# Kernel optimization log

Hardware: AMD Instinct MI355X
Metric: run time of the kernel (lower is better)

The kernel has to match this reference:

```python
import jax, jax.numpy as jnp
import numpy as np
import math

B, S, E = 2, 2048, 1024
H, HD = 16, 64
FF = 4 * E
EPS = float(jnp.finfo(jnp.float32).eps)  # torch nn.RMSNorm default eps


def setup_inputs() -> dict:
    key = jax.random.key(0)
    ks = jax.random.split(key, 20)
    sd = 0.02
    inp = {
        "x": jax.random.normal(ks[0], (B, S, E), jnp.float32),
        "wq": jax.random.normal(ks[1], (E, H * HD), jnp.float32) * sd,
        "bq": jnp.zeros((H * HD,), jnp.float32),
        "wk": jax.random.normal(ks[2], (E, HD), jnp.float32) * sd,
        "bk": jnp.zeros((HD,), jnp.float32),
        "wv": jax.random.normal(ks[3], (E, HD), jnp.float32) * sd,
        "bv": jnp.zeros((HD,), jnp.float32),
        "wo": jax.random.normal(ks[4], (H * HD, E), jnp.float32) * sd,
        "bo": jnp.zeros((E,), jnp.float32),
        "wg": jax.random.normal(ks[5], (E, FF), jnp.float32) * sd,
        "bg": jnp.zeros((FF,), jnp.float32),
        "wu": jax.random.normal(ks[6], (E, FF), jnp.float32) * sd,
        "bu": jnp.zeros((FF,), jnp.float32),
        "wd": jax.random.normal(ks[7], (FF, E), jnp.float32) * sd,
        "bd": jnp.zeros((E,), jnp.float32),
        "g1": jnp.ones((E,), jnp.float32),
        "g2": jnp.ones((E,), jnp.float32),
    }
    return inp


def rmsnorm(x, g):
    ms = jnp.mean(jnp.square(x), axis=-1, keepdims=True)
    return x * jax.lax.rsqrt(ms + EPS) * g


def apply_rope(t):
    # t: [B, H, S, D]; llama-style rotate-half, theta=10000, start_pos=0
    d = t.shape[-1]
    half = d // 2
    inv_freq = 1.0 / (10000.0 ** (jnp.arange(half, dtype=jnp.float32) / half))
    pos = jnp.arange(t.shape[2], dtype=jnp.float32)
    ang = pos[:, None] * inv_freq[None, :]  # [S, half]
    cos, sin = jnp.cos(ang), jnp.sin(ang)
    t1, t2 = t[..., :half], t[..., half:]
    return jnp.concatenate([t1 * cos - t2 * sin, t1 * sin + t2 * cos], axis=-1)


def decoder_fwd(x, wq, bq, wk, bk, wv, bv, wo, bo, wg, bg, wu, bu, wd, bd, g1, g2):
    residual = x
    h = rmsnorm(x, g1)
    # MQA projections: H query heads, 1 shared K/V head
    q = (h @ wq + bq).reshape(B, S, H, HD).transpose(0, 2, 1, 3)  # [B,H,S,D]
    k = (h @ wk + bk)[:, None]                                    # [B,1,S,D]
    v = (h @ wv + bv)                                             # [B,S,D]
    q = apply_rope(q)
    k = apply_rope(k)[:, 0]                                       # [B,S,D]
    scores = jnp.einsum("bhqd,bkd->bhqk", q, k) / math.sqrt(HD)
    causal = jnp.tril(jnp.ones((S, S), dtype=bool))
    scores = jnp.where(causal, scores, -jnp.inf)
    attn = jax.nn.softmax(scores, axis=-1)
    out = jnp.einsum("bhqk,bkd->bhqd", attn, v)
    out = out.transpose(0, 2, 1, 3).reshape(B, S, H * HD)
    x = (out @ wo + bo) + residual
    residual = x
    h = rmsnorm(x, g2)
    gated = jax.nn.gelu(h @ wg + bg, approximate=False)  # torch GELU is exact erf
    up = h @ wu + bu
    x = (up * gated) @ wd + bd
    return x + residual


def reference(x, wq, bq, wk, bk, wv, bv, wo, bo, wg, bg, wu, bu, wd, bd, g1, g2):
    return decoder_fwd(x, wq, bq, wk, bk, wv, bv, wo, bo, wg, bg, wu, bu, wd, bd, g1, g2)
```

## Files before the change

### kernel.cpp

```cpp
#include <hip/hip_runtime.h>
#include <hip/hip_bf16.h>
#include <math.h>

#define BB 2
#define SS 2048
#define EE 1024
#define HH 16
#define HD 64
#define FFF 4096
#define MROWS (BB * SS)
#define EPS_F 1.1920929e-7f
#define NQKV 1152

typedef __hip_bfloat16 bf16;
typedef __attribute__((ext_vector_type(8))) short short8;
typedef __attribute__((ext_vector_type(4))) short short4v;
typedef __attribute__((ext_vector_type(4))) float floatx4;

typedef const __attribute__((address_space(1))) void* gas_t;
typedef __attribute__((address_space(3))) void* las_t;

#define BAR __builtin_amdgcn_s_barrier()
#define WLG do { asm volatile("s_waitcnt lgkmcnt(0)" ::: "memory"); \
                 __builtin_amdgcn_sched_barrier(0); } while (0)
#define VMC(N) asm volatile("s_waitcnt vmcnt(" #N ")" ::: "memory")

__global__ __launch_bounds__(256) void rmsnorm_kernel(const float* __restrict__ x,
                                                      const float* __restrict__ g,
                                                      bf16* __restrict__ out,
                                                      int cols) {
    int row = blockIdx.x;
    const float* xr = x + (size_t)row * cols;
    float ss = 0.0f;
    for (int c = threadIdx.x; c < cols; c += 256) {
        float v = xr[c];
        ss += v * v;
    }
    for (int off = 32; off > 0; off >>= 1) ss += __shfl_xor(ss, off, 64);
    __shared__ float red[4];
    int wave = threadIdx.x >> 6;
    if ((threadIdx.x & 63) == 0) red[wave] = ss;
    __syncthreads();
    float tot = red[0] + red[1] + red[2] + red[3];
    float rs = rsqrtf(tot / (float)cols + EPS_F);
    bf16* orow = out + (size_t)row * cols;
    for (int c = threadIdx.x; c < cols; c += 256) {
        orow[c] = __float2bfloat16(xr[c] * rs * g[c]);
    }
}

__device__ __forceinline__ void transpose_tile32(const float* __restrict__ W,
                                                 bf16* __restrict__ Wt,
                                                 int K, int N, int bx, int by,
                                                 int tid, float (*t)[33]) {
    int n0 = bx * 32, k0 = by * 32;
    int tx = tid & 31, ty = tid >> 5;
#pragma unroll
    for (int i = 0; i < 4; ++i) {
        int kk = ty + i * 8;
        t[kk][tx] = W[(size_t)(k0 + kk) * N + n0 + tx];
    }
    __syncthreads();
#pragma unroll
    for (int i = 0; i < 4; ++i) {
        int nn = ty + i * 8;
        Wt[(size_t)(n0 + nn) * K + k0 + tx] = __float2bfloat16(t[tx][nn]);
    }
}

__global__ __launch_bounds__(256) void prep_weights_kernel(
        const float* __restrict__ wq, const float* __restrict__ wk,
        const float* __restrict__ wv, const float* __restrict__ wo,
        const float* __restrict__ bq, const float* __restrict__ bk,
        const float* __restrict__ bv,
        bf16* __restrict__ wqkvT, bf16* __restrict__ woT,
        float* __restrict__ bqkv, float* __restrict__ ct, float* __restrict__ st) {
    __shared__ float t[32][33];
    int bid = blockIdx.x, tid = threadIdx.x;
    if (bid < 1024) {
        transpose_tile32(wq, wqkvT, EE, EE, bid & 31, bid >> 5, tid, t);
    } else if (bid < 1088) {
        int b2 = bid - 1024;
        transpose_tile32(wk, wqkvT + (size_t)1024 * EE, EE, HD, b2 & 1, b2 >> 1, tid, t);
    } else if (bid < 1152) {
        int b2 = bid - 1088;
        transpose_tile32(wv, wqkvT + (size_t)1088 * EE, EE, HD, b2 & 1, b2 >> 1, tid, t);
    } else if (bid < 2176) {
        int b2 = bid - 1152;
        transpose_tile32(wo, woT, EE, EE, b2 & 31, b2 >> 5, tid, t);
    } else if (bid < 2432) {
        int idx = (bid - 2176) * 256 + tid;
        int i = idx & 31, s = idx >> 5;
        float inv = powf(10000.0f, -(float)i / 32.0f);
        float ang = (float)s * inv;
        ct[idx] = cosf(ang);
        st[idx] = sinf(ang);
    } else {
        int tt = (bid - 2432) * 256 + tid;
        if (tt < NQKV) {
            float v;
            if (tt < 1024)      v = bq[tt];
            else if (tt < 1088) v = bk[tt - 1024];
            else                v = bv[tt - 1088];
            bqkv[tt] = v;
        }
    }
}

__global__ __launch_bounds__(256) void ffn_weights_kernel(
        const float* __restrict__ wg, const float* __restrict__ wu,
        const float* __restrict__ wd,
        bf16* __restrict__ wgT, bf16* __restrict__ wuT, bf16* __restrict__ wdT) {
    __shared__ float t[32][33];
    int bid = blockIdx.x, tid = threadIdx.x;
    if (bid < 4096) {
        transpose_tile32(wg, wgT, EE, FFF, bid & 127, bid >> 7, tid, t);
    } else if (bid < 8192) {
        int b2 = bid - 4096;
        transpose_tile32(wu, wuT, EE, FFF, b2 & 127, b2 >> 7, tid, t);
    } else {
        int b2 = bid - 8192;
        transpose_tile32(wd, wdT, FFF, EE, b2 & 31, b2 >> 5, tid, t);
    }
}

#define GK 64

__global__ __launch_bounds__(256) void gemm_qkv_kernel(
        const bf16* __restrict__ A, const bf16* __restrict__ Bt,
        const float* __restrict__ bias,
        const float* __restrict__ ct, const float* __restrict__ st,
        bf16* __restrict__ qout, bf16* __restrict__ kout,
        bf16* __restrict__ vout, int K) {
    __shared__ short As[128 * GK];
    __shared__ short Bs[128 * GK];
    int tid = threadIdx.x;
    int wave = tid >> 6, lane = tid & 63;
    int wm = (wave >> 1) * 64, wn = (wave & 1) * 64;
    int row0 = blockIdx.y * 128, col0 = blockIdx.x * 128;
    int lr = lane & 15, lq = lane >> 4;

    int srow = wave * 32 + (lane >> 3);
    int scol = (lane & 7) * 8;
    const bf16* Abase = A + (size_t)(row0 + srow) * K + scol;
    const bf16* Bbase = Bt + (size_t)(col0 + srow) * K + scol;

    floatx4 acc[4][4];
#pragma unroll
    for (int mi = 0; mi < 4; ++mi)
#pragma unroll
        for (int ni = 0; ni < 4; ++ni)
            acc[mi][ni] = (floatx4){0.f, 0.f, 0.f, 0.f};

    for (int k0 = 0; k0 < K; k0 += GK) {
        __syncthreads();
#pragma unroll
        for (int c = 0; c < 4; ++c) {
            __builtin_amdgcn_global_load_lds(
                (gas_t)(Abase + (size_t)(c * 8) * K + k0),
                (las_t)&As[(wave * 32 + c * 8) * GK], 16, 0, 0);
            __builtin_amdgcn_global_load_lds(
                (gas_t)(Bbase + (size_t)(c * 8) * K + k0),
                (las_t)&Bs[(wave * 32 + c * 8) * GK], 16, 0, 0);
        }
        __syncthreads();
#pragma unroll
        for (int ks = 0; ks < GK; ks += 32) {
            short8 af[4], bfr[4];
#pragma unroll
            for (int mi = 0; mi < 4; ++mi)
                af[mi] = *(const short8*)&As[(wm + mi * 16 + lr) * GK + ks + lq * 8];
#pragma unroll
            for (int ni = 0; ni < 4; ++ni)
                bfr[ni] = *(const short8*)&Bs[(wn + ni * 16 + lr) * GK + ks + lq * 8];
#pragma unroll
            for (int mi = 0; mi < 4; ++mi)
#pragma unroll
                for (int ni = 0; ni < 4; ++ni)
                    acc[mi][ni] = __builtin_amdgcn_mfma_f32_16x16x32_bf16(
                        af[mi], bfr[ni], acc[mi][ni], 0, 0, 0);
        }
    }

    int hcol = col0 + wn;
    if (hcol < 1088) {
        bool isQ = hcol < 1024;
#pragma unroll
        for (int mi = 0; mi < 4; ++mi) {
#pragma unroll
            for (int ni = 0; ni < 2; ++ni) {
                int i = ni * 16 + lr;
                float b1 = bias[hcol + i];
                float b2 = bias[hcol + i + 32];
#pragma unroll
                for (int r = 0; r < 4; ++r) {
                    int gr = row0 + wm + mi * 16 + lq * 4 + r;
                    int s = gr & (SS - 1);
                    float c  = ct[s * 32 + i];
                    float sn = st[s * 32 + i];
                    float t1 = acc[mi][ni][r] + b1;
                    float t2 = acc[mi][ni + 2][r] + b2;
                    float o1 = t1 * c - t2 * sn;
                    float o2 = t1 * sn + t2 * c;
                    if (isQ) {
                        qout[(size_t)gr * 1024 + hcol + i]      = __float2bfloat16(o1 * 0.125f);
                        qout[(size_t)gr * 1024 + hcol + i + 32] = __float2bfloat16(o2 * 0.125f);
                    } else {
                        kout[(size_t)gr * 64 + i]      = __float2bfloat16(o1);
                        kout[(size_t)gr * 64 + i + 32] = __float2bfloat16(o2);
                    }
                }
            }
        }
    } else {
#pragma unroll
        for (int mi = 0; mi < 4; ++mi)
#pragma unroll
            for (int ni = 0; ni < 4; ++ni) {
                int vcol = ni * 16 + lr;
                float bv_ = bias[1088 + vcol];
#pragma unroll
                for (int r = 0; r < 4; ++r) {
                    int gr = row0 + wm + mi * 16 + lq * 4 + r;
                    vout[(size_t)gr * 64 + vcol] = __float2bfloat16(acc[mi][ni][r] + bv_);
                }
            }
    }
}

__global__ __launch_bounds__(256) void gemm_n64_kernel(
        const bf16* __restrict__ A, const bf16* __restrict__ Bt,
        const float* __restrict__ bias, const float* __restrict__ aux,
        float* __restrict__ C, int M, int N, int K) {
    __shared__ short As[128 * GK];
    __shared__ short Bs[64 * GK];
    int tid = threadIdx.x;
    int wave = tid >> 6, lane = tid & 63;
    int wm = wave * 32;
    int row0 = blockIdx.y * 128, col0 = blockIdx.x * 64;
    int lr = lane & 15, lq = lane >> 4;

    int srow = (lane >> 3);
    int scol = (lane & 7) * 8;
    const bf16* Abase = A + (size_t)(row0 + wave * 32 + srow) * K + scol;
    const bf16* Bbase = Bt + (size_t)(col0 + wave * 16 + srow) * K + scol;

    floatx4 acc[2][4];
#pragma unroll
    for (int mi = 0; mi < 2; ++mi)
#pragma unroll
        for (int ni = 0; ni < 4; ++ni)
            acc[mi][ni] = (floatx4){0.f, 0.f, 0.f, 0.f};

    for (int k0 = 0; k0 < K; k0 += GK) {
        __syncthreads();
#pragma unroll
        for (int c = 0; c < 4; ++c)
            __builtin_amdgcn_global_load_lds(
                (gas_t)(Abase + (size_t)(c * 8) * K + k0),
                (las_t)&As[(wave * 32 + c * 8) * GK], 16, 0, 0);
#pragma unroll
        for (int c = 0; c < 2; ++c)
            __builtin_amdgcn_global_load_lds(
                (gas_t)(Bbase + (size_t)(c * 8) * K + k0),
                (las_t)&Bs[(wave * 16 + c * 8) * GK], 16, 0, 0);
        __syncthreads();
#pragma unroll
        for (int ks = 0; ks < GK; ks += 32) {
            short8 af[2], bfr[4];
#pragma unroll
            for (int mi = 0; mi < 2; ++mi)
                af[mi] = *(const short8*)&As[(wm + mi * 16 + lr) * GK + ks + lq * 8];
#pragma unroll
            for (int ni = 0; ni < 4; ++ni)
                bfr[ni] = *(const short8*)&Bs[(ni * 16 + lr) * GK + ks + lq * 8];
#pragma unroll
            for (int mi = 0; mi < 2; ++mi)
#pragma unroll
                for (int ni = 0; ni < 4; ++ni)
                    acc[mi][ni] = __builtin_amdgcn_mfma_f32_16x16x32_bf16(
                        af[mi], bfr[ni], acc[mi][ni], 0, 0, 0);
        }
    }

#pragma unroll
    for (int mi = 0; mi < 2; ++mi) {
#pragma unroll
        for (int ni = 0; ni < 4; ++ni) {
            int gc = col0 + ni * 16 + lr;
            float bv = bias[gc];
#pragma unroll
            for (int r = 0; r < 4; ++r) {
                int gr = row0 + wm + mi * 16 + lq * 4 + r;
                size_t idx = (size_t)gr * N + gc;
                C[idx] = acc[mi][ni][r] + bv + aux[idx];
            }
        }
    }
}

#define FFN_RD_A(KH, MH) \
    { const short* Ap = &Ab[buf][KH][0]; \
      af[0] = *(const short8*)&Ap[(wr * 128 + ((MH) * 4 + 0) * 16 + lr) * 32 + cs8]; \
      af[1] = *(const short8*)&Ap[(wr * 128 + ((MH) * 4 + 1) * 16 + lr) * 32 + cs8]; \
      af[2] = *(const short8*)&Ap[(wr * 128 + ((MH) * 4 + 2) * 16 + lr) * 32 + cs8]; \
      af[3] = *(const short8*)&Ap[(wr * 128 + ((MH) * 4 + 3) * 16 + lr) * 32 + cs8]; }

#define FFN_RD_B(KH) \
    { const short* Bp = &Bb[buf][KH][0]; \
      gf[0] = *(const short8*)&Bp[(wc * 32 + lr) * 32 + cs8]; \
      gf[1] = *(const short8*)&Bp[(wc * 32 + 16 + lr) * 32 + cs8]; \
      uf[0] = *(const short8*)&Bp[4096 + (wc * 32 + lr) * 32 + cs8]; \
      uf[1] = *(const short8*)&Bp[4096 + (wc * 32 + 16 + lr) * 32 + cs8]; }

#define FFN_MM(MH) \
    __builtin_amdgcn_s_setprio(1); \
    { _Pragma("unroll") for (int mi = 0; mi < 4; ++mi) { \
        ag[(MH) * 4 + mi][0] = __builtin_amdgcn_mfma_f32_16x16x32_bf16(af[mi], gf[0], ag[(MH) * 4 + mi][0], 0, 0, 0); \
        ag[(MH) * 4 + mi][1] = __builtin_amdgcn_mfma_f32_16x16x32_bf16(af[mi], gf[1], ag[(MH) * 4 + mi][1], 0, 0, 0); \
        au[(MH) * 4 + mi][0] = __builtin_amdgcn_mfma_f32_16x16x32_bf16(af[mi], uf[0], au[(MH) * 4 + mi][0], 0, 0, 0); \
        au[(MH) * 4 + mi][1] = __builtin_amdgcn_mfma_f32_16x16x32_bf16(af[mi], uf[1], au[(MH) * 4 + mi][1], 0, 0, 0); } } \
    __builtin_amdgcn_s_setprio(0);

__global__ __launch_bounds__(512, 2) void gemm_ffn_kernel(
        const bf16* __restrict__ A, const bf16* __restrict__ Bg,
        const bf16* __restrict__ Bu, const float* __restrict__ biasg,
        const float* __restrict__ biasu, bf16* __restrict__ C, int K) {
    __shared__ short Ab[2][2][8192];
    __shared__ short Bb[2][2][8192];

    const int tid = threadIdx.x;
    const int w = tid >> 6, lane = tid & 63;
    const int wr = w >> 2, wc = w & 3;
    const int lr = lane & 15, quad = lane >> 4;
    const int row0 = blockIdx.y * 256, col0 = blockIdx.x * 128;
    const int NT = K >> 6;
    const int cs8 = (quad ^ ((lr >> 1) & 3)) * 8;

    const int sr = tid >> 2;
    const int scs = (((tid & 3) ^ ((tid >> 3) & 3))) * 8;

    auto stageA = [&](short* dst, int kcol) {
        __builtin_amdgcn_global_load_lds(
            (gas_t)(A + (size_t)(row0 + sr) * K + kcol + scs),
            (las_t)(dst + tid * 8), 16, 0, 0);
        __builtin_amdgcn_global_load_lds(
            (gas_t)(A + (size_t)(row0 + 128 + sr) * K + kcol + scs),
            (las_t)(dst + 4096 + tid * 8), 16, 0, 0);
    };
    auto stageB = [&](short* dst, int kcol) {
        __builtin_amdgcn_global_load_lds(
            (gas_t)(Bg + (size_t)(col0 + sr) * K + kcol + scs),
            (las_t)(dst + tid * 8), 16, 0, 0);
        __builtin_amdgcn_global_load_lds(
            (gas_t)(Bu + (size_t)(col0 + sr) * K + kcol + scs),
            (las_t)(dst + 4096 + tid * 8), 16, 0, 0);
    };

    floatx4 ag[8][2], au[8][2];
#pragma unroll
    for (int mi = 0; mi < 8; ++mi)
#pragma unroll
        for (int ni = 0; ni < 2; ++ni) {
            ag[mi][ni] = (floatx4){0.f, 0.f, 0.f, 0.f};
            au[mi][ni] = (floatx4){0.f, 0.f, 0.f, 0.f};
        }

    stageA(&Ab[0][0][0], 0);
    stageB(&Bb[0][0][0], 0);
    stageA(&Ab[0][1][0], 32);
    stageB(&Bb[0][1][0], 32);
    stageA(&Ab[1][0][0], 64);
    stageB(&Bb[1][0][0], 64);
    VMC(8);
    BAR;

    for (int k = 0; k < NT; ++k) {
        const int buf = k & 1;
        short8 gf[2], uf[2];
        {
            short8 af[4];
            FFN_RD_A(0, 0)
            FFN_RD_B(0)
            if (k + 1 < NT) stageA(&Ab[buf ^ 1][1][0], (k + 1) * 64 + 32);
            BAR; WLG;
            FFN_MM(0)
            BAR;
        }
        {
            short8 af[4];
            FFN_RD_A(0, 1)
            if (k + 1 < NT) stageB(&Bb[buf ^ 1][1][0], (k + 1) * 64 + 32);
            BAR; WLG;
            FFN_MM(1)
            if (k < NT - 1) { VMC(8); } else { VMC(0); }
            BAR;
        }
        {
            short8 af[4];
            FFN_RD_A(1, 0)
            FFN_RD_B(1)
            if (k + 2 < NT) stageA(&Ab[buf][0][0], (k + 2) * 64);
            BAR; WLG;
            FFN_MM(0)
            BAR;
        }
        {
            short8 af[4];
            FFN_RD_A(1, 1)
            if (k + 2 < NT) stageB(&Bb[buf][0][0], (k + 2) * 64);
            BAR; WLG;
            FFN_MM(1)
            if (k < NT - 2) { VMC(8); } else if (k == NT - 2) { VMC(4); }
            BAR;
        }
    }

#pragma unroll
    for (int mi = 0; mi < 8; ++mi) {
#pragma unroll
        for (int ni = 0; ni < 2; ++ni) {
            int gc = col0 + wc * 32 + ni * 16 + lr;
            float bg_ = biasg[gc], bu_ = biasu[gc];
#pragma unroll
            for (int r = 0; r < 4; ++r) {
                int gr = row0 + wr * 128 + mi * 16 + quad * 4 + r;
                float g = ag[mi][ni][r] + bg_;
                float u = au[mi][ni][r] + bu_;
                float v = 0.5f * g * (1.0f + erff(g * 0.70710678118654752f)) * u;
                C[(size_t)gr * FFF + gc] = __float2bfloat16(v);
            }
        }
    }
}

__global__ __launch_bounds__(256) void prep_v_kernel(const bf16* __restrict__ vb,
                                                     bf16* __restrict__ vtb) {
    __shared__ short t[64][65];
    int s0 = blockIdx.x * 64, b = blockIdx.y;
    int tid = threadIdx.x;
    const short* vs = (const short*)vb;
    short* vd = (short*)vtb;
    for (int i = tid; i < 4096; i += 256) {
        int s = i >> 6, d = i & 63;
        t[d][s] = vs[((size_t)(b * SS + s0 + s)) * 64 + d];
    }
    __syncthreads();
    for (int i = tid; i < 4096; i += 256) {
        int d = i >> 6, sl = i & 63;
        vd[((size_t)(b * 64 + d)) * SS + s0 + sl] = t[d][sl];
    }
}

#define PST 68
#define SM_SHIFT 6.0f

__global__ __launch_bounds__(256, 3) void attn_mfma_kernel(
        const bf16* __restrict__ q, const bf16* __restrict__ kb,
        const bf16* __restrict__ vt,
        float* __restrict__ O0p, float* __restrict__ O1p,
        float* __restrict__ l0p, float* __restrict__ l1p) {
    __shared__ short Kb_s[2][64 * 64];
    __shared__ short Vb_s[2][64 * 64];
    __shared__ short Ps[4][16 * PST];

    int h = blockIdx.y, b = blockIdx.z;
    int px = blockIdx.x >> 1, half = blockIdx.x & 1;
    int tid = threadIdx.x, w = tid >> 6, lane = tid & 63;
    int lr = lane & 15, quad = lane >> 4;
    int rsw = lane & 7;

    float* __restrict__ Op = half ? O1p : O0p;
    float* __restrict__ lp = half ? l1p : l0p;

    const bf16* kbB = kb + (size_t)b * SS * 64;
    const bf16* vtB = vt + (size_t)b * 64 * SS;

    int st_sub = lane >> 3;
    int st_col = ((lane & 7) ^ st_sub) << 3;

    auto stage_tile = [&](int nxt, int j0s) {
#pragma unroll
        for (int i = 0; i < 2; ++i) {
            int rr = i * 32 + w * 8 + st_sub;
            __builtin_amdgcn_global_load_lds(
                (gas_t)(kbB + (size_t)(j0s + rr) * 64 + st_col),
                (las_t)&Kb_s[nxt][(i * 256 + w * 64) * 8], 16, 0, 0);
            __builtin_amdgcn_global_load_lds(
                (gas_t)(vtB + (size_t)rr * SS + j0s + st_col),
                (las_t)&Vb_s[nxt][(i * 256 + w * 64) * 8], 16, 0, 0);
        }
    };

    for (int pass = 0; pass < 2; ++pass) {
        int qt = (pass == 0) ? px : (SS / 64 - 1 - px);
        int q0 = qt * 64;

        const bf16* qrow = q + ((size_t)(b * SS + q0 + w * 16 + lr)) * (HH * HD) + h * HD;
        short8 qf0 = *(const short8*)(qrow + quad * 8);
        short8 qf1 = *(const short8*)(qrow + 32 + quad * 8);

        int n  = qt + 1;
        int n0 = (n + 1) >> 1;
        int tlo = half ? n0 : 0;
        int thi = half ? n  : n0;

        floatx4 O[4];
#pragma unroll
        for (int ni = 0; ni < 4; ++ni) O[ni] = (floatx4){0.f, 0.f, 0.f, 0.f};
        float lrow[4] = {0.f, 0.f, 0.f, 0.f};

        int cur = 0;
        if (tlo < thi) stage_tile(0, tlo * 64);
        __syncthreads();

        for (int t = tlo; t < thi; ++t) {
            if (t + 1 < thi) stage_tile(cur ^ 1, (t + 1) * 64);

            int j0 = t * 64;

            floatx4 S[4];
#pragma unroll
            for (int ni = 0; ni < 4; ++ni) S[ni] = (floatx4){0.f, 0.f, 0.f, 0.f};
#pragma unroll
            for (int ni = 0; ni < 4; ++ni) {
                const short* Kc = &Kb_s[cur][(ni * 16 + lr) * 64];
                short8 b0 = *(const short8*)&Kc[(quad ^ rsw) * 8];
                short8 b1 = *(const short8*)&Kc[((quad ^ rsw) ^ 4) * 8];
                S[ni] = __builtin_amdgcn_mfma_f32_16x16x32_bf16(qf0, b0, S[ni], 0, 0, 0);
                S[ni] = __builtin_amdgcn_mfma_f32_16x16x32_bf16(qf1, b1, S[ni], 0, 0, 0);
            }

            short8 vf[8];
#pragma unroll
            for (int ni = 0; ni < 4; ++ni) {
                const short* Vc = &Vb_s[cur][(ni * 16 + lr) * 64];
                vf[2 * ni]     = *(const short8*)&Vc[(quad ^ rsw) * 8];
                vf[2 * ni + 1] = *(const short8*)&Vc[((quad ^ rsw) ^ 4) * 8];
            }

            if (t == qt) {
                int rowg = q0 + w * 16 + quad * 4;
#pragma unroll
                for (int ni = 0; ni < 4; ++ni) {
                    int colg = j0 + ni * 16 + lr;
#pragma unroll
                    for (int r = 0; r < 4; ++r)
                        if (colg > rowg + r) S[ni][r] = -3.0e38f;
                }
            }

#pragma unroll
            for (int ni = 0; ni < 4; ++ni)
#pragma unroll
                for (int r = 0; r < 4; ++r)
                    S[ni][r] = __expf(S[ni][r] - SM_SHIFT);
#pragma unroll
            for (int r = 0; r < 4; ++r)
                lrow[r] += S[0][r] + S[1][r] + S[2][r] + S[3][r];

#pragma unroll
            for (int ni = 0; ni < 4; ++ni)
#pragma unroll
                for (int r = 0; r < 4; ++r) {
                    bf16 pb = __float2bfloat16(S[ni][r]);
                    Ps[w][(quad * 4 + r) * PST + ni * 16 + lr] = *(short*)&pb;
                }
            short4v a0 = *(const short4v*)&Ps[w][lr * PST + quad * 8];
            short4v a1 = *(const short4v*)&Ps[w][lr * PST + quad * 8 + 4];
            short4v a2 = *(const short4v*)&Ps[w][lr * PST + 32 + quad * 8];
            short4v a3 = *(const short4v*)&Ps[w][lr * PST + 32 + quad * 8 + 4];
            short8 p0 = __builtin_shufflevector(a0, a1, 0, 1, 2, 3, 4, 5, 6, 7);
            short8 p1 = __builtin_shufflevector(a2, a3, 0, 1, 2, 3, 4, 5, 6, 7);

#pragma unroll
            for (int ni = 0; ni < 4; ++ni) {
                O[ni] = __builtin_amdgcn_mfma_f32_16x16x32_bf16(p0, vf[2 * ni], O[ni], 0, 0, 0);
                O[ni] = __builtin_amdgcn_mfma_f32_16x16x32_bf16(p1, vf[2 * ni + 1], O[ni], 0, 0, 0);
            }

            __syncthreads();
            cur ^= 1;
        }

#pragma unroll
        for (int r = 0; r < 4; ++r) {
            float l = lrow[r];
            for (int off = 1; off < 16; off <<= 1) l += __shfl_xor(l, off, 64);
            lrow[r] = l;
        }

#pragma unroll
        for (int ni = 0; ni < 4; ++ni) {
            int gc = h * 64 + ni * 16 + lr;
#pragma unroll
            for (int r = 0; r < 4; ++r) {
                int gr = b * SS + q0 + w * 16 + quad * 4 + r;
                Op[(size_t)gr * (HH * HD) + gc] = O[ni][r];
            }
        }
        if (lr == 0) {
#pragma unroll
            for (int r = 0; r < 4; ++r) {
                int gr = b * SS + q0 + w * 16 + quad * 4 + r;
                lp[(size_t)gr * HH + h] = lrow[r];
            }
        }
    }
}

__global__ __launch_bounds__(256) void attn_combine_kernel(
        const float* __restrict__ O0p, const float* __restrict__ O1p,
        const float* __restrict__ l0p, const float* __restrict__ l1p,
        bf16* __restrict__ o) {
    int idx = blockIdx.x * 256 + threadIdx.x;
    int d4  = idx & 15;
    int hh  = (idx >> 4) & 15;
    int row = idx >> 8;
    float l = l0p[row * HH + hh] + l1p[row * HH + hh];
    float inv = 1.0f / l;
    size_t base = (size_t)row * (HH * HD) + hh * 64 + d4 * 4;
    float4 a = *(const float4*)(O0p + base);
    float4 c = *(const float4*)(O1p + base);
    short4v o4;
    {
        bf16 v0 = __float2bfloat16((a.x + c.x) * inv);
        bf16 v1 = __float2bfloat16((a.y + c.y) * inv);
        bf16 v2 = __float2bfloat16((a.z + c.z) * inv);
        bf16 v3 = __float2bfloat16((a.w + c.w) * inv);
        o4[0] = *(short*)&v0; o4[1] = *(short*)&v1;
        o4[2] = *(short*)&v2; o4[3] = *(short*)&v3;
    }
    *(short4v*)(o + base) = o4;
}

#define MB (1024ull * 1024ull)

extern "C" void kernel_launch(void* const* d_in, const int* in_sizes, int n_in,
                              void* d_out, int out_size, void* d_ws, size_t ws_size,
                              hipStream_t stream) {
    const float* x  = (const float*)d_in[0];
    const float* wq = (const float*)d_in[1];
    const float* bq = (const float*)d_in[2];
    const float* wk = (const float*)d_in[3];
    const float* bk = (const float*)d_in[4];
    const float* wv = (const float*)d_in[5];
    const float* bv = (const float*)d_in[6];
    const float* wo = (const float*)d_in[7];
    const float* bo = (const float*)d_in[8];
    const float* wg = (const float*)d_in[9];
    const float* bg = (const float*)d_in[10];
    const float* wu = (const float*)d_in[11];
    const float* bu = (const float*)d_in[12];
    const float* wd = (const float*)d_in[13];
    const float* bd = (const float*)d_in[14];
    const float* g1 = (const float*)d_in[15];
    const float* g2 = (const float*)d_in[16];
    float* out = (float*)d_out;

    char* ws = (char*)d_ws;
    bf16*  qbf   = (bf16*)(ws);
    bf16*  wuT   = (bf16*)(ws + 8 * MB);
    float* x2    = (float*)(ws + 16 * MB);
    bf16*  h1b   = (bf16*)(ws + 32 * MB);
    bf16*  vb    = (bf16*)(ws + 40 * MB);
    bf16*  ao    = (bf16*)(ws + 42 * MB);
    bf16*  gg    = (bf16*)(ws + 50 * MB);
    bf16*  kbf   = (bf16*)(ws + 50 * MB);
    bf16*  vtb   = (bf16*)(ws + 50 * MB + 512 * 1024);
    float* Opart0 = (float*)(ws + 16 * MB);
    float* Opart1 = (float*)(ws + 51 * MB);
    float* lpart0 = (float*)(ws + 67 * MB);
    float* lpart1 = (float*)(ws + 67 * MB + 256 * 1024);
    float* ctab   = (float*)(ws + 68 * MB);
    float* stab   = (float*)(ws + 68 * MB + 256 * 1024);
    bf16*  wqkvT = (bf16*)(ws + 82 * MB);
    float* bqkv  = (float*)(ws + 84 * MB + 512 * 1024);
    bf16*  woT   = (bf16*)(ws + 85 * MB);
    bf16*  wgT   = (bf16*)(ws);
    bf16*  wdT   = (bf16*)(ws + 42 * MB);
    bf16*  h2b   = h1b;

    prep_weights_kernel<<<2437, 256, 0, stream>>>(
        wq, wk, wv, wo, bq, bk, bv, wqkvT, woT, bqkv, ctab, stab);

    rmsnorm_kernel<<<MROWS, 256, 0, stream>>>(x, g1, h1b, EE);

    gemm_qkv_kernel<<<dim3(NQKV / 128, MROWS / 128), 256, 0, stream>>>(
        h1b, wqkvT, bqkv, ctab, stab, qbf, kbf, vb, EE);

    prep_v_kernel<<<dim3(SS / 64, BB), 256, 0, stream>>>(vb, vtb);

    attn_mfma_kernel<<<dim3(2 * SS / 128, HH, BB), 256, 0, stream>>>(
        qbf, kbf, vtb, Opart0, Opart1, lpart0, lpart1);
    attn_combine_kernel<<<(MROWS * HH * HD / 4) / 256, 256, 0, stream>>>(
        Opart0, Opart1, lpart0, lpart1, ao);

    gemm_n64_kernel<<<dim3(EE / 64, MROWS / 128), 256, 0, stream>>>(
        ao, woT, bo, x, x2, MROWS, EE, EE);

    rmsnorm_kernel<<<MROWS, 256, 0, stream>>>(x2, g2, h2b, EE);

    ffn_weights_kernel<<<12288, 256, 0, stream>>>(wg, wu, wd, wgT, wuT, wdT);

    gemm_ffn_kernel<<<dim3(FFF / 128, MROWS / 256), 512, 0, stream>>>(
        h2b, wgT, wuT, bg, bu, gg, EE);

    gemm_n64_kernel<<<dim3(EE / 64, MROWS / 128), 256, 0, stream>>>(
        gg, wdT, bd, x2, out, MROWS, EE, FFF);
}
```

Measured before the change: 415.3 us.

## Split-K the QKV, output and down-projection GEMMs and vectorize RMSNorm

The QKV GEMM, the attention output projection and the FFN down projection now split K in half across blockIdx.z. This doubles the number of workgroups so more of the GPU's compute units are busy on these modest grids. Partial fp32 results go to workspace buffers and are merged by a new combine kernel (which applies bias and RoPE for QKV) or an in-place add kernel. RMSNorm switches to one float4 load and one packed bf16 store per thread. The cost is extra fp32 partial-sum traffic to memory and two or three extra kernel launches.

After: 419.5 us. Within noise of the previous version (+1.0%).

```diff
diff --git a/kernel.cpp b/kernel.cpp
--- a/kernel.cpp
+++ b/kernel.cpp
@@ -29,24 +29,28 @@
                                                       const float* __restrict__ g,
                                                       bf16* __restrict__ out,
                                                       int cols) {
-    int row = blockIdx.x;
-    const float* xr = x + (size_t)row * cols;
-    float ss = 0.0f;
-    for (int c = threadIdx.x; c < cols; c += 256) {
-        float v = xr[c];
-        ss += v * v;
-    }
+    int row = blockIdx.x, tid = threadIdx.x;
+    const float4* xr = (const float4*)(x + (size_t)row * cols);
+    float4 v = xr[tid];
+    float ss = v.x * v.x + v.y * v.y + v.z * v.z + v.w * v.w;
     for (int off = 32; off > 0; off >>= 1) ss += __shfl_xor(ss, off, 64);
     __shared__ float red[4];
-    int wave = threadIdx.x >> 6;
-    if ((threadIdx.x & 63) == 0) red[wave] = ss;
+    int wave = tid >> 6;
+    if ((tid & 63) == 0) red[wave] = ss;
     __syncthreads();
     float tot = red[0] + red[1] + red[2] + red[3];
     float rs = rsqrtf(tot / (float)cols + EPS_F);
-    bf16* orow = out + (size_t)row * cols;
-    for (int c = threadIdx.x; c < cols; c += 256) {
-        orow[c] = __float2bfloat16(xr[c] * rs * g[c]);
-    }
+    float4 gv = ((const float4*)g)[tid];
+    short4v o;
+    {
+        bf16 b0 = __float2bfloat16(v.x * rs * gv.x);
+        bf16 b1 = __float2bfloat16(v.y * rs * gv.y);
+        bf16 b2 = __float2bfloat16(v.z * rs * gv.z);
+        bf16 b3 = __float2bfloat16(v.w * rs * gv.w);
+        o[0] = *(short*)&b0; o[1] = *(short*)&b1;
+        o[2] = *(short*)&b2; o[3] = *(short*)&b3;
+    }
+    *(short4v*)(out + (size_t)row * cols + tid * 4) = o;
 }
 
 __device__ __forceinline__ void transpose_tile32(const float* __restrict__ W,
@@ -128,10 +132,7 @@
 
 __global__ __launch_bounds__(256) void gemm_qkv_kernel(
         const bf16* __restrict__ A, const bf16* __restrict__ Bt,
-        const float* __restrict__ bias,
-        const float* __restrict__ ct, const float* __restrict__ st,
-        bf16* __restrict__ qout, bf16* __restrict__ kout,
-        bf16* __restrict__ vout, int K) {
+        float* __restrict__ p0, float* __restrict__ p1, int K) {
     __shared__ short As[128 * GK];
     __shared__ short Bs[128 * GK];
     int tid = threadIdx.x;
@@ -139,6 +140,8 @@
     int wm = (wave >> 1) * 64, wn = (wave & 1) * 64;
     int row0 = blockIdx.y * 128, col0 = blockIdx.x * 128;
     int lr = lane & 15, lq = lane >> 4;
+    int kh = blockIdx.z;
+    int kbeg = kh * (K >> 1), kend = kbeg + (K >> 1);
 
     int srow = wave * 32 + (lane >> 3);
     int scol = (lane & 7) * 8;
@@ -152,7 +155,7 @@
         for (int ni = 0; ni < 4; ++ni)
             acc[mi][ni] = (floatx4){0.f, 0.f, 0.f, 0.f};
 
-    for (int k0 = 0; k0 < K; k0 += GK) {
+    for (int k0 = kbeg; k0 < kend; k0 += GK) {
         __syncthreads();
 #pragma unroll
         for (int c = 0; c < 4; ++c) {
@@ -182,56 +185,59 @@
         }
     }
 
-    int hcol = col0 + wn;
-    if (hcol < 1088) {
-        bool isQ = hcol < 1024;
-#pragma unroll
-        for (int mi = 0; mi < 4; ++mi) {
-#pragma unroll
-            for (int ni = 0; ni < 2; ++ni) {
-                int i = ni * 16 + lr;
-                float b1 = bias[hcol + i];
-                float b2 = bias[hcol + i + 32];
-#pragma unroll
-                for (int r = 0; r < 4; ++r) {
-                    int gr = row0 + wm + mi * 16 + lq * 4 + r;
-                    int s = gr & (SS - 1);
-                    float c  = ct[s * 32 + i];
-                    float sn = st[s * 32 + i];
-                    float t1 = acc[mi][ni][r] + b1;
-                    float t2 = acc[mi][ni + 2][r] + b2;
-                    float o1 = t1 * c - t2 * sn;
-                    float o2 = t1 * sn + t2 * c;
-                    if (isQ) {
-                        qout[(size_t)gr * 1024 + hcol + i]      = __float2bfloat16(o1 * 0.125f);
-                        qout[(size_t)gr * 1024 + hcol + i + 32] = __float2bfloat16(o2 * 0.125f);
-                    } else {
-                        kout[(size_t)gr * 64 + i]      = __float2bfloat16(o1);
-                        kout[(size_t)gr * 64 + i + 32] = __float2bfloat16(o2);
-                    }
-                }
-            }
+    float* __restrict__ P = kh ? p1 : p0;
+#pragma unroll
+    for (int mi = 0; mi < 4; ++mi)
+#pragma unroll
+        for (int ni = 0; ni < 4; ++ni) {
+            int gc = col0 + wn + ni * 16 + lr;
+#pragma unroll
+            for (int r = 0; r < 4; ++r) {
+                int gr = row0 + wm + mi * 16 + lq * 4 + r;
+                P[(size_t)gr * NQKV + gc] = acc[mi][ni][r];
+            }
+        }
+}
+
+__global__ __launch_bounds__(192) void qkv_combine_kernel(
+        const float* __restrict__ p0, const float* __restrict__ p1,
+        const float* __restrict__ bias, const float* __restrict__ ct,
+        const float* __restrict__ st, bf16* __restrict__ qout,
+        bf16* __restrict__ kout, bf16* __restrict__ vout) {
+    int row = blockIdx.y;
+    int j = blockIdx.x * 192 + threadIdx.x;
+    const float* r0 = p0 + (size_t)row * NQKV;
+    const float* r1 = p1 + (size_t)row * NQKV;
+    int s = row & (SS - 1);
+    if (j < 544) {
+        int i, col1;
+        if (j < 512) { i = j & 31; col1 = (j >> 5) * 64 + i; }
+        else         { i = j - 512; col1 = 1024 + i; }
+        int col2 = col1 + 32;
+        float t1 = r0[col1] + r1[col1] + bias[col1];
+        float t2 = r0[col2] + r1[col2] + bias[col2];
+        float c = ct[s * 32 + i], sn = st[s * 32 + i];
+        float o1 = t1 * c - t2 * sn;
+        float o2 = t1 * sn + t2 * c;
+        if (j < 512) {
+            qout[(size_t)row * 1024 + col1]      = __float2bfloat16(o1 * 0.125f);
+            qout[(size_t)row * 1024 + col1 + 32] = __float2bfloat16(o2 * 0.125f);
+        } else {
+            kout[(size_t)row * 64 + i]      = __float2bfloat16(o1);
+            kout[(size_t)row * 64 + i + 32] = __float2bfloat16(o2);
         }
     } else {
-#pragma unroll
-        for (int mi = 0; mi < 4; ++mi)
-#pragma unroll
-            for (int ni = 0; ni < 4; ++ni) {
-                int vcol = ni * 16 + lr;
-                float bv_ = bias[1088 + vcol];
-#pragma unroll
-                for (int r = 0; r < 4; ++r) {
-                    int gr = row0 + wm + mi * 16 + lq * 4 + r;
-                    vout[(size_t)gr * 64 + vcol] = __float2bfloat16(acc[mi][ni][r] + bv_);
-                }
-            }
-    }
-}
-
-__global__ __launch_bounds__(256) void gemm_n64_kernel(
+        int i = (j - 544) * 2;
+        int col = 1088 + i;
+        vout[(size_t)row * 64 + i]     = __float2bfloat16(r0[col] + r1[col] + bias[col]);
+        vout[(size_t)row * 64 + i + 1] = __float2bfloat16(r0[col + 1] + r1[col + 1] + bias[col + 1]);
+    }
+}
+
+__global__ __launch_bounds__(256) void gemm_n64_split_kernel(
         const bf16* __restrict__ A, const bf16* __restrict__ Bt,
         const float* __restrict__ bias, const float* __restrict__ aux,
-        float* __restrict__ C, int M, int N, int K) {
+        float* __restrict__ C, float* __restrict__ P, int N, int K) {
     __shared__ short As[128 * GK];
     __shared__ short Bs[64 * GK];
     int tid = threadIdx.x;
@@ -239,6 +245,8 @@
     int wm = wave * 32;
     int row0 = blockIdx.y * 128, col0 = blockIdx.x * 64;
     int lr = lane & 15, lq = lane >> 4;
+    int kh = blockIdx.z;
+    int kbeg = kh * (K >> 1), kend = kbeg + (K >> 1);
 
     int srow = (lane >> 3);
     int scol = (lane & 7) * 8;
@@ -252,7 +260,7 @@
         for (int ni = 0; ni < 4; ++ni)
             acc[mi][ni] = (floatx4){0.f, 0.f, 0.f, 0.f};
 
-    for (int k0 = 0; k0 < K; k0 += GK) {
+    for (int k0 = kbeg; k0 < kend; k0 += GK) {
         __syncthreads();
 #pragma unroll
         for (int c = 0; c < 4; ++c)
@@ -293,10 +301,20 @@
             for (int r = 0; r < 4; ++r) {
                 int gr = row0 + wm + mi * 16 + lq * 4 + r;
                 size_t idx = (size_t)gr * N + gc;
-                C[idx] = acc[mi][ni][r] + bv + aux[idx];
-            }
-        }
-    }
+                if (kh == 0) C[idx] = acc[mi][ni][r] + bv + aux[idx];
+                else         P[idx] = acc[mi][ni][r];
+            }
+        }
+    }
+}
+
+__global__ __launch_bounds__(256) void add_inplace_kernel(
+        float* __restrict__ C, const float* __restrict__ P) {
+    int idx = blockIdx.x * 256 + threadIdx.x;
+    float4 c = ((const float4*)C)[idx];
+    float4 p = ((const float4*)P)[idx];
+    c.x += p.x; c.y += p.y; c.z += p.z; c.w += p.w;
+    ((float4*)C)[idx] = c;
 }
 
 #define FFN_RD_A(KH, MH) \
@@ -659,7 +677,9 @@
     float* out = (float*)d_out;
 
     char* ws = (char*)d_ws;
+    float* pbuf  = (float*)(ws);
     bf16*  qbf   = (bf16*)(ws);
+    float* p1q   = (float*)(ws + 8 * MB);
     bf16*  wuT   = (bf16*)(ws + 8 * MB);
     float* x2    = (float*)(ws + 16 * MB);
     bf16*  h1b   = (bf16*)(ws + 32 * MB);
@@ -668,12 +688,13 @@
     bf16*  gg    = (bf16*)(ws + 50 * MB);
     bf16*  kbf   = (bf16*)(ws + 50 * MB);
     bf16*  vtb   = (bf16*)(ws + 50 * MB + 512 * 1024);
+    float* p0q   = (float*)(ws + 51 * MB);
     float* Opart0 = (float*)(ws + 16 * MB);
     float* Opart1 = (float*)(ws + 51 * MB);
     float* lpart0 = (float*)(ws + 67 * MB);
     float* lpart1 = (float*)(ws + 67 * MB + 256 * 1024);
-    float* ctab   = (float*)(ws + 68 * MB);
-    float* stab   = (float*)(ws + 68 * MB + 256 * 1024);
+    float* ctab   = (float*)(ws + 70 * MB);
+    float* stab   = (float*)(ws + 70 * MB + 256 * 1024);
     bf16*  wqkvT = (bf16*)(ws + 82 * MB);
     float* bqkv  = (float*)(ws + 84 * MB + 512 * 1024);
     bf16*  woT   = (bf16*)(ws + 85 * MB);
@@ -686,8 +707,11 @@
 
     rmsnorm_kernel<<<MROWS, 256, 0, stream>>>(x, g1, h1b, EE);
 
-    gemm_qkv_kernel<<<dim3(NQKV / 128, MROWS / 128), 256, 0, stream>>>(
-        h1b, wqkvT, bqkv, ctab, stab, qbf, kbf, vb, EE);
+    gemm_qkv_kernel<<<dim3(NQKV / 128, MROWS / 128, 2), 256, 0, stream>>>(
+        h1b, wqkvT, p0q, p1q, EE);
+
+    qkv_combine_kernel<<<dim3(3, MROWS), 192, 0, stream>>>(
+        p0q, p1q, bqkv, ctab, stab, qbf, kbf, vb);
 
     prep_v_kernel<<<dim3(SS / 64, BB), 256, 0, stream>>>(vb, vtb);
 
@@ -696,8 +720,9 @@
     attn_combine_kernel<<<(MROWS * HH * HD / 4) / 256, 256, 0, stream>>>(
         Opart0, Opart1, lpart0, lpart1, ao);
 
-    gemm_n64_kernel<<<dim3(EE / 64, MROWS / 128), 256, 0, stream>>>(
-        ao, woT, bo, x, x2, MROWS, EE, EE);
+    gemm_n64_split_kernel<<<dim3(EE / 64, MROWS / 128, 2), 256, 0, stream>>>(
+        ao, woT, bo, x, x2, pbuf, EE, EE);
+    add_inplace_kernel<<<(MROWS * EE / 4) / 256, 256, 0, stream>>>(x2, pbuf);
 
     rmsnorm_kernel<<<MROWS, 256, 0, stream>>>(x2, g2, h2b, EE);
 
@@ -706,6 +731,7 @@
     gemm_ffn_kernel<<<dim3(FFF / 128, MROWS / 256), 512, 0, stream>>>(
         h2b, wgT, wuT, bg, bu, gg, EE);
 
-    gemm_n64_kernel<<<dim3(EE / 64, MROWS / 128), 256, 0, stream>>>(
-        gg, wdT, bd, x2, out, MROWS, EE, FFF);
-}
+    gemm_n64_split_kernel<<<dim3(EE / 64, MROWS / 128, 2), 256, 0, stream>>>(
+        gg, wdT, bd, x2, out, pbuf, EE, FFF);
+    add_inplace_kernel<<<(MROWS * EE / 4) / 256, 256, 0, stream>>>(out, pbuf);
+}
```
